# Performance work log

Hardware: AMD Instinct MI355X
Metric: run time of the kernel (lower is better)

Reference implementation:

```python
import jax, jax.numpy as jnp
import numpy as np

B, S, H = 128, 512, 768      # batch, seq, encoder hidden
NL = 42                      # len(LABEL_TO_ID)
LD = 300                     # label_dim
DK, DV = 64, 768             # K_dim, V_dim
HID = 768                    # opt['hidden_dim']
P = 512                      # max_seq_length == pos_indicator
INF = 1e12                   # constant.INFINITY_NUMBER
NEG = -1e9


def gelu(x):
    return 0.5 * x * (1.0 + jax.lax.erf(x * 0.7071067811865476))


def setup_inputs() -> dict:
    key = jax.random.key(0)
    ks = jax.random.split(key, 24)
    sc = 0.02
    return {
        "inputs": jax.random.normal(ks[0], (B, S, H), jnp.float32),
        "pos_ids": jax.random.randint(ks[1], (B, S), 0, 53),
        "dep_ids": jax.random.randint(ks[2], (B, S), 0, 42),
        "subj_pos": jax.random.randint(ks[3], (B, S), 0, P + 1),
        "obj_pos": jax.random.randint(ks[4], (B, S), 0, P + 1),
        "adj": jnp.zeros((1, 1, 1), jnp.float32),  # unused by forward
        # stacked per-label Q/K projections (41 = NL-1 labels, label 0 excluded)
        "WQ": jax.random.normal(ks[5], (NL - 1, DK, H), jnp.float32) * sc,
        "bQ": jax.random.normal(ks[6], (NL - 1, DK), jnp.float32) * sc,
        "WK": jax.random.normal(ks[7], (NL - 1, DK, LD), jnp.float32) * sc,
        "bK": jax.random.normal(ks[8], (NL - 1, DK), jnp.float32) * sc,
        "WV_w": jax.random.normal(ks[9], (DV, H), jnp.float32) * sc,
        "WV_b": jax.random.normal(ks[10], (DV,), jnp.float32) * sc,
        "Wout_w": jax.random.normal(ks[11], (H, DV), jnp.float32) * sc,
        "Wout_b": jax.random.normal(ks[12], (H,), jnp.float32) * sc,
        "ln_g": jnp.ones((H,), jnp.float32),
        "ln_b": jnp.zeros((H,), jnp.float32),
        "label_emb": jax.random.normal(ks[13], (NL, LD), jnp.float32) * sc,
        "feat_w": jax.random.normal(ks[14], (HID, 3 * H), jnp.float32) * sc,
        "feat_b": jax.random.normal(ks[15], (HID,), jnp.float32) * sc,
        "out_w": jax.random.normal(ks[16], (LD, HID), jnp.float32) * sc,
        "out_b": jax.random.normal(ks[17], (LD,), jnp.float32) * sc,
    }


def reference(inputs, pos_ids, dep_ids, subj_pos, obj_pos, adj,
              WQ, bQ, WK, bK, WV_w, WV_b, Wout_w, Wout_b, ln_g, ln_b,
              label_emb, feat_w, feat_b, out_w, out_b):
    dt = inputs.dtype
    # combined attention mask (bool OR, as torch bool+bool): entity markers + padding
    mask = (subj_pos == P) | (obj_pos == P) | (pos_ids == 0)   # [B,S]

    # --- LabelAttention: 41-loop collapses to one fused projection ---
    lab = label_emb[1:NL]                                      # [41,LD] labels 1..41
    kvec = jnp.einsum('ld,lkd->lk', lab, WK) + bK              # [41,DK] per-label keys
    # scores_sum[b,s] = sum_l (x W_Q_l^T + b_Q_l) . k_l  /sqrt(dk)  + 41*mask*NEG
    w_eff = jnp.einsum('lk,lkh->h', kvec, WQ)                  # [H]
    c = jnp.sum(kvec * bQ)                                     # scalar
    scores = (inputs @ w_eff + c) / 8.0                        # sqrt(DK)=8; [B,S]
    scores = scores + (NL - 1) * mask.astype(dt) * NEG
    attn = jax.nn.softmax(scores, axis=-1)                     # [B,S]

    wv = inputs @ WV_w.T + WV_b                                # [B,S,DV]
    ctx = jnp.einsum('bs,bsd->bd', attn, wv)                   # [B,DV]
    ctx = gelu(ctx @ Wout_w.T + Wout_b)                        # [B,H]
    mu = ctx.mean(-1, keepdims=True)
    var = ((ctx - mu) ** 2).mean(-1, keepdims=True)
    ctx = (ctx - mu) / jnp.sqrt(var + 1e-5) * ln_g + ln_b

    # --- entity max pooling (mask True where NOT part of entity) ---
    sm = (subj_pos != P)[:, :, None]
    om = (obj_pos != P)[:, :, None]
    subj_out = jnp.where(sm, -INF, inputs).max(axis=1)         # [B,H]
    obj_out = jnp.where(om, -INF, inputs).max(axis=1)          # [B,H]

    feats = jnp.concatenate([subj_out, obj_out, ctx], axis=-1)  # [B,3H]
    feats = gelu(feats @ feat_w.T + feat_b)                     # [B,HID]
    feats = gelu(feats @ out_w.T + out_b)                       # [B,LD]

    logits = feats @ label_emb.T                                # [B,42]
    return logits, ctx
```

## Files before the change

### kernel.cpp

```cpp
#include <hip/hip_runtime.h>
#include <math.h>

#define BB 128
#define SS 512
#define HH 768
#define PPOS 512
#define NEGC (-1.0e9f)
#define NINF (-1.0e12f)

#define OFF_KVEC   0
#define OFF_WEFF   2624
#define OFF_C      3392
#define OFF_SCORES 4096
#define OFF_CAT    0
#define OFF_POOLED 294912
#define OFF_PP     393216
#define OFF_PS     786432
#define OFF_PO     1179648
#define OFF_CTXA   393216
#define OFF_CTXB   491520
#define OFF_F1     589824
#define OFF_F2     688128

__device__ __forceinline__ float gelu_f(float x) {
    return 0.5f * x * (1.0f + erff(x * 0.70710678118654752f));
}
__device__ __forceinline__ float dot4(float4 a, float4 b) {
    return a.x*b.x + a.y*b.y + a.z*b.z + a.w*b.w;
}

template<int K4, int ACT>
__global__ __launch_bounds__(256) void k_mm(const float* __restrict__ A,
        const float* __restrict__ W, const float* __restrict__ bias,
        float* __restrict__ C, int M, int N) {
    int lane = threadIdx.x & 63;
    int wave = (blockIdx.x * 256 + threadIdx.x) >> 6;
    int ntn = (N + 15) >> 4;
    int m0 = (wave / ntn) << 2;
    if (m0 >= M) return;
    int n0 = ((wave % ntn) << 4) + (lane >> 2);
    int ks = lane & 3;
    bool nvalid = (n0 < N);
    const float4* A4 = (const float4*)A;
    const float4* w_row = (const float4*)W + (size_t)(nvalid ? n0 : 0) * K4;
    const float4* a0 = A4 + (size_t)m0 * K4;
    const float4* a1 = a0 + K4;
    const float4* a2 = a1 + K4;
    const float4* a3 = a2 + K4;
    float acc0 = 0.f, acc1 = 0.f, acc2 = 0.f, acc3 = 0.f;
    #pragma unroll 4
    for (int j = ks; j < K4; j += 4) {
        float4 wv = w_row[j];
        acc0 += dot4(a0[j], wv);
        acc1 += dot4(a1[j], wv);
        acc2 += dot4(a2[j], wv);
        acc3 += dot4(a3[j], wv);
    }
    acc0 += __shfl_xor(acc0, 1, 64); acc0 += __shfl_xor(acc0, 2, 64);
    acc1 += __shfl_xor(acc1, 1, 64); acc1 += __shfl_xor(acc1, 2, 64);
    acc2 += __shfl_xor(acc2, 1, 64); acc2 += __shfl_xor(acc2, 2, 64);
    acc3 += __shfl_xor(acc3, 1, 64); acc3 += __shfl_xor(acc3, 2, 64);
    if (ks == 0 && nvalid) {
        float b = bias ? bias[n0] : 0.f;
        float v0 = acc0 + b, v1 = acc1 + b, v2 = acc2 + b, v3 = acc3 + b;
        if (ACT == 1) { v0 = gelu_f(v0); v1 = gelu_f(v1); v2 = gelu_f(v2); v3 = gelu_f(v3); }
        C[(size_t)m0 * N + n0] = v0;
        C[(size_t)(m0 + 1) * N + n0] = v1;
        C[(size_t)(m0 + 2) * N + n0] = v2;
        C[(size_t)(m0 + 3) * N + n0] = v3;
    }
}

__global__ __launch_bounds__(256) void k_kvec2(const float* __restrict__ label_emb,
        const float* __restrict__ WK, const float* __restrict__ bK,
        float* __restrict__ ws) {
    if (blockIdx.x < 3) ws[OFF_WEFF + blockIdx.x * 256 + threadIdx.x] = 0.f;
    if (blockIdx.x == 3 && threadIdx.x == 0) ws[OFF_C] = 0.f;
    int lane = threadIdx.x & 63;
    int idx = (blockIdx.x * 256 + threadIdx.x) >> 6;
    int l = idx >> 6;
    const float4* lab4 = (const float4*)(label_emb + (size_t)(l + 1) * 300);
    const float4* wk4  = (const float4*)(WK + (size_t)idx * 300);
    float acc = dot4(lab4[lane], wk4[lane]);
    if (lane < 11) acc += dot4(lab4[64 + lane], wk4[64 + lane]);
    #pragma unroll
    for (int off = 32; off > 0; off >>= 1) acc += __shfl_xor(acc, off, 64);
    if (lane == 0) ws[OFF_KVEC + idx] = acc + bK[idx];
}

__global__ __launch_bounds__(256) void k_weff2(const float* __restrict__ WQ,
        const float* __restrict__ bQ, float* __restrict__ ws) {
    int lane = threadIdx.x & 63;
    int w = (blockIdx.x * 256 + threadIdx.x) >> 6;
    if (w < 492) {
        int jc = w / 12, hg = w % 12;
        int h = hg * 64 + lane;
        const float* wq = WQ + (size_t)(jc * 64) * HH + h;
        const float* kv = ws + OFF_KVEC + jc * 64;
        float acc = 0.f;
        #pragma unroll 8
        for (int j = 0; j < 64; ++j) acc += kv[j] * wq[(size_t)j * HH];
        atomicAdd(&ws[OFF_WEFF + h], acc);
    } else if (w == 492) {
        float acc = 0.f;
        for (int j = lane; j < 2624; j += 64) acc += ws[OFF_KVEC + j] * bQ[j];
        #pragma unroll
        for (int off = 32; off > 0; off >>= 1) acc += __shfl_xor(acc, off, 64);
        if (lane == 0) atomicAdd(&ws[OFF_C], acc);
    }
}

__global__ __launch_bounds__(256) void k_scores(const float* __restrict__ inputs,
        const int* __restrict__ pos_ids, const int* __restrict__ subj_pos,
        const int* __restrict__ obj_pos, float* __restrict__ ws) {
    int wave = threadIdx.x >> 6, lane = threadIdx.x & 63;
    const float4* in4 = (const float4*)inputs;
    const float4* w4  = (const float4*)(ws + OFF_WEFF);
    float c = ws[OFF_C];
    float4 w0 = w4[lane], w1 = w4[64 + lane], w2 = w4[128 + lane];
    int wid = blockIdx.x * 4 + wave;
    for (int i = 0; i < 8; ++i) {
        int row = wid + 8192 * i;
        const float4* r4 = in4 + (size_t)row * 192;
        float acc = dot4(r4[lane], w0) + dot4(r4[64 + lane], w1) + dot4(r4[128 + lane], w2);
        #pragma unroll
        for (int off = 32; off > 0; off >>= 1) acc += __shfl_down(acc, off, 64);
        if (lane == 0) {
            bool m = (subj_pos[row] == PPOS) | (obj_pos[row] == PPOS) | (pos_ids[row] == 0);
            float sc = (acc + c) * 0.125f;
            if (m) sc += 41.0f * NEGC;
            ws[OFF_SCORES + row] = sc;
        }
    }
}

__global__ void k_softmax(float* __restrict__ ws) {
    __shared__ float red[256];
    int b = blockIdx.x, t = threadIdx.x;
    float* sc = ws + OFF_SCORES + (size_t)b * SS;
    float v0 = sc[t], v1 = sc[t + 256];
    red[t] = fmaxf(v0, v1); __syncthreads();
    for (int s2 = 128; s2 > 0; s2 >>= 1) {
        if (t < s2) red[t] = fmaxf(red[t], red[t + s2]);
        __syncthreads();
    }
    float m = red[0]; __syncthreads();
    float e0 = expf(v0 - m), e1 = expf(v1 - m);
    red[t] = e0 + e1; __syncthreads();
    for (int s2 = 128; s2 > 0; s2 >>= 1) {
        if (t < s2) red[t] += red[t + s2];
        __syncthreads();
    }
    float inv = 1.0f / red[0];
    sc[t] = e0 * inv; sc[t + 256] = e1 * inv;
}

__global__ __launch_bounds__(192) void k_pool(const float* __restrict__ inputs,
        const int* __restrict__ subj_pos, const int* __restrict__ obj_pos,
        float* __restrict__ ws) {
    __shared__ float la[128];
    __shared__ int lsf[128];
    __shared__ int lof[128];
    int chunk = blockIdx.x, b = blockIdx.y, t = threadIdx.x;
    int s0 = chunk * 128;
    if (t < 128) {
        int gs = b * SS + s0 + t;
        la[t]  = ws[OFF_SCORES + gs];
        lsf[t] = (subj_pos[gs] == PPOS);
        lof[t] = (obj_pos[gs] == PPOS);
    }
    __syncthreads();
    const float4* in4 = (const float4*)inputs;
    float4 pool = make_float4(0.f, 0.f, 0.f, 0.f);
    float4 smax = make_float4(NINF, NINF, NINF, NINF);
    float4 omax = make_float4(NINF, NINF, NINF, NINF);
    for (int s = 0; s < 128; ++s) {
        float4 x = in4[((size_t)(b * SS + s0 + s)) * 192 + t];
        float a = la[s];
        pool.x += a * x.x; pool.y += a * x.y; pool.z += a * x.z; pool.w += a * x.w;
        if (lsf[s]) {
            smax.x = fmaxf(smax.x, x.x); smax.y = fmaxf(smax.y, x.y);
            smax.z = fmaxf(smax.z, x.z); smax.w = fmaxf(smax.w, x.w);
        }
        if (lof[s]) {
            omax.x = fmaxf(omax.x, x.x); omax.y = fmaxf(omax.y, x.y);
            omax.z = fmaxf(omax.z, x.z); omax.w = fmaxf(omax.w, x.w);
        }
    }
    size_t o = (size_t)(b * 4 + chunk) * 192 + t;
    ((float4*)(ws + OFF_PP))[o] = pool;
    ((float4*)(ws + OFF_PS))[o] = smax;
    ((float4*)(ws + OFF_PO))[o] = omax;
}

__global__ void k_reduce(float* __restrict__ ws) {
    int i = blockIdx.x * 256 + threadIdx.x;
    int b = i / HH, h = i - b * HH;
    float p = 0.f, sm = NINF, om = NINF;
    for (int j = 0; j < 4; ++j) {
        int o = (b * 4 + j) * HH + h;
        p += ws[OFF_PP + o];
        sm = fmaxf(sm, ws[OFF_PS + o]);
        om = fmaxf(om, ws[OFF_PO + o]);
    }
    ws[OFF_POOLED + i] = p;
    ws[OFF_CAT + (size_t)b * 2304 + h] = sm;
    ws[OFF_CAT + (size_t)b * 2304 + 768 + h] = om;
}

__global__ void k_ln(const float* __restrict__ ln_g, const float* __restrict__ ln_b,
                     float* __restrict__ ws, float* __restrict__ out) {
    __shared__ float red[256];
    __shared__ float red2[256];
    int b = blockIdx.x, t = threadIdx.x;
    const float* x = ws + OFF_CTXB + (size_t)b * HH;
    float a0 = x[t], a1 = x[t + 256], a2 = x[t + 512];
    red[t]  = a0 + a1 + a2;
    red2[t] = a0 * a0 + a1 * a1 + a2 * a2;
    __syncthreads();
    for (int s2 = 128; s2 > 0; s2 >>= 1) {
        if (t < s2) { red[t] += red[t + s2]; red2[t] += red2[t + s2]; }
        __syncthreads();
    }
    float mu  = red[0] * (1.0f / 768.0f);
    float var = red2[0] * (1.0f / 768.0f) - mu * mu;
    float inv = rsqrtf(var + 1e-5f);
    float* o = out + 5376 + (size_t)b * HH;
    float* cc = ws + OFF_CAT + (size_t)b * 2304 + 1536;
    float r0 = (a0 - mu) * inv * ln_g[t]       + ln_b[t];
    float r1 = (a1 - mu) * inv * ln_g[t + 256] + ln_b[t + 256];
    float r2 = (a2 - mu) * inv * ln_g[t + 512] + ln_b[t + 512];
    o[t] = r0; o[t + 256] = r1; o[t + 512] = r2;
    cc[t] = r0; cc[t + 256] = r1; cc[t + 512] = r2;
}

extern "C" void kernel_launch(void* const* d_in, const int* in_sizes, int n_in,
                              void* d_out, int out_size, void* d_ws, size_t ws_size,
                              hipStream_t stream) {
    const float* inputs    = (const float*)d_in[0];
    const int*   pos_ids   = (const int*)d_in[1];
    const int*   subj_pos  = (const int*)d_in[3];
    const int*   obj_pos   = (const int*)d_in[4];
    const float* WQ        = (const float*)d_in[6];
    const float* bQ        = (const float*)d_in[7];
    const float* WK        = (const float*)d_in[8];
    const float* bK        = (const float*)d_in[9];
    const float* WV_w      = (const float*)d_in[10];
    const float* WV_b      = (const float*)d_in[11];
    const float* Wout_w    = (const float*)d_in[12];
    const float* Wout_b    = (const float*)d_in[13];
    const float* ln_g      = (const float*)d_in[14];
    const float* ln_b      = (const float*)d_in[15];
    const float* label_emb = (const float*)d_in[16];
    const float* feat_w    = (const float*)d_in[17];
    const float* feat_b    = (const float*)d_in[18];
    const float* out_w     = (const float*)d_in[19];
    const float* out_b     = (const float*)d_in[20];
    float* out = (float*)d_out;
    float* ws  = (float*)d_ws;

    k_kvec2  <<<656, 256, 0, stream>>>(label_emb, WK, bK, ws);
    k_weff2  <<<124, 256, 0, stream>>>(WQ, bQ, ws);
    k_scores <<<2048, 256, 0, stream>>>(inputs, pos_ids, subj_pos, obj_pos, ws);
    k_softmax<<<BB, 256, 0, stream>>>(ws);
    k_pool   <<<dim3(4, BB), 192, 0, stream>>>(inputs, subj_pos, obj_pos, ws);
    k_reduce <<<384, 256, 0, stream>>>(ws);
    k_mm<192,0><<<384, 256, 0, stream>>>(ws + OFF_POOLED, WV_w, WV_b, ws + OFF_CTXA, BB, HH);
    k_mm<192,1><<<384, 256, 0, stream>>>(ws + OFF_CTXA, Wout_w, Wout_b, ws + OFF_CTXB, BB, HH);
    k_ln     <<<BB, 256, 0, stream>>>(ln_g, ln_b, ws, out);
    k_mm<576,1><<<384, 256, 0, stream>>>(ws + OFF_CAT, feat_w, feat_b, ws + OFF_F1, BB, HH);
    k_mm<192,1><<<152, 256, 0, stream>>>(ws + OFF_F1, out_w, out_b, ws + OFF_F2, BB, 300);
    k_mm<75,0><<<24, 256, 0, stream>>>(ws + OFF_F2, label_emb, nullptr, out, BB, 42);
}
```

Baseline: 540.0 us.

## Fuse softmax into pooling, split pooling finer, halve matmul row tile

```diff
diff --git a/kernel.cpp b/kernel.cpp
--- a/kernel.cpp
+++ b/kernel.cpp
@@ -15,8 +15,8 @@
 #define OFF_CAT    0
 #define OFF_POOLED 294912
 #define OFF_PP     393216
-#define OFF_PS     786432
-#define OFF_PO     1179648
+#define OFF_PS     1179648
+#define OFF_PO     1966080
 #define OFF_CTXA   393216
 #define OFF_CTXB   491520
 #define OFF_F1     589824
@@ -29,45 +29,43 @@
     return a.x*b.x + a.y*b.y + a.z*b.z + a.w*b.w;
 }
 
-template<int K4, int ACT>
+template<int K4, int ACT, int MT>
 __global__ __launch_bounds__(256) void k_mm(const float* __restrict__ A,
         const float* __restrict__ W, const float* __restrict__ bias,
         float* __restrict__ C, int M, int N) {
     int lane = threadIdx.x & 63;
     int wave = (blockIdx.x * 256 + threadIdx.x) >> 6;
     int ntn = (N + 15) >> 4;
-    int m0 = (wave / ntn) << 2;
+    int m0 = (wave / ntn) * MT;
     if (m0 >= M) return;
     int n0 = ((wave % ntn) << 4) + (lane >> 2);
     int ks = lane & 3;
     bool nvalid = (n0 < N);
     const float4* A4 = (const float4*)A;
     const float4* w_row = (const float4*)W + (size_t)(nvalid ? n0 : 0) * K4;
-    const float4* a0 = A4 + (size_t)m0 * K4;
-    const float4* a1 = a0 + K4;
-    const float4* a2 = a1 + K4;
-    const float4* a3 = a2 + K4;
-    float acc0 = 0.f, acc1 = 0.f, acc2 = 0.f, acc3 = 0.f;
+    const float4* ar = A4 + (size_t)m0 * K4;
+    float acc[MT];
+    #pragma unroll
+    for (int r = 0; r < MT; ++r) acc[r] = 0.f;
     #pragma unroll 4
     for (int j = ks; j < K4; j += 4) {
         float4 wv = w_row[j];
-        acc0 += dot4(a0[j], wv);
-        acc1 += dot4(a1[j], wv);
-        acc2 += dot4(a2[j], wv);
-        acc3 += dot4(a3[j], wv);
-    }
-    acc0 += __shfl_xor(acc0, 1, 64); acc0 += __shfl_xor(acc0, 2, 64);
-    acc1 += __shfl_xor(acc1, 1, 64); acc1 += __shfl_xor(acc1, 2, 64);
-    acc2 += __shfl_xor(acc2, 1, 64); acc2 += __shfl_xor(acc2, 2, 64);
-    acc3 += __shfl_xor(acc3, 1, 64); acc3 += __shfl_xor(acc3, 2, 64);
+        #pragma unroll
+        for (int r = 0; r < MT; ++r) acc[r] += dot4(ar[(size_t)r * K4 + j], wv);
+    }
+    #pragma unroll
+    for (int r = 0; r < MT; ++r) {
+        acc[r] += __shfl_xor(acc[r], 1, 64);
+        acc[r] += __shfl_xor(acc[r], 2, 64);
+    }
     if (ks == 0 && nvalid) {
         float b = bias ? bias[n0] : 0.f;
-        float v0 = acc0 + b, v1 = acc1 + b, v2 = acc2 + b, v3 = acc3 + b;
-        if (ACT == 1) { v0 = gelu_f(v0); v1 = gelu_f(v1); v2 = gelu_f(v2); v3 = gelu_f(v3); }
-        C[(size_t)m0 * N + n0] = v0;
-        C[(size_t)(m0 + 1) * N + n0] = v1;
-        C[(size_t)(m0 + 2) * N + n0] = v2;
-        C[(size_t)(m0 + 3) * N + n0] = v3;
+        #pragma unroll
+        for (int r = 0; r < MT; ++r) {
+            float v = acc[r] + b;
+            if (ACT == 1) v = gelu_f(v);
+            C[(size_t)(m0 + r) * N + n0] = v;
+        }
     }
 }
 
@@ -134,38 +132,39 @@
     }
 }
 
-__global__ void k_softmax(float* __restrict__ ws) {
+__global__ __launch_bounds__(192) void k_pool(const float* __restrict__ inputs,
+        const int* __restrict__ subj_pos, const int* __restrict__ obj_pos,
+        float* __restrict__ ws) {
     __shared__ float red[256];
-    int b = blockIdx.x, t = threadIdx.x;
-    float* sc = ws + OFF_SCORES + (size_t)b * SS;
-    float v0 = sc[t], v1 = sc[t + 256];
-    red[t] = fmaxf(v0, v1); __syncthreads();
+    __shared__ float al[64];
+    __shared__ int lsf[64];
+    __shared__ int lof[64];
+    int chunk = blockIdx.x, b = blockIdx.y, t = threadIdx.x;
+    int s0 = chunk * 64;
+    const float* sc = ws + OFF_SCORES + (size_t)b * SS;
+    float v0 = sc[t], v1 = sc[t + 192], v2 = (t < 128) ? sc[t + 384] : NINF;
+    red[t] = fmaxf(fmaxf(v0, v1), v2);
+    if (t >= 128) { }
+    if (t < 64) red[t + 192] = NINF;
+    __syncthreads();
     for (int s2 = 128; s2 > 0; s2 >>= 1) {
         if (t < s2) red[t] = fmaxf(red[t], red[t + s2]);
         __syncthreads();
     }
-    float m = red[0]; __syncthreads();
-    float e0 = expf(v0 - m), e1 = expf(v1 - m);
-    red[t] = e0 + e1; __syncthreads();
+    float m = red[0];
+    __syncthreads();
+    float e0 = expf(v0 - m) + expf(v1 - m) + ((t < 128) ? expf(v2 - m) : 0.f);
+    red[t] = e0;
+    if (t < 64) red[t + 192] = 0.f;
+    __syncthreads();
     for (int s2 = 128; s2 > 0; s2 >>= 1) {
         if (t < s2) red[t] += red[t + s2];
         __syncthreads();
     }
     float inv = 1.0f / red[0];
-    sc[t] = e0 * inv; sc[t + 256] = e1 * inv;
-}
-
-__global__ __launch_bounds__(192) void k_pool(const float* __restrict__ inputs,
-        const int* __restrict__ subj_pos, const int* __restrict__ obj_pos,
-        float* __restrict__ ws) {
-    __shared__ float la[128];
-    __shared__ int lsf[128];
-    __shared__ int lof[128];
-    int chunk = blockIdx.x, b = blockIdx.y, t = threadIdx.x;
-    int s0 = chunk * 128;
-    if (t < 128) {
+    if (t < 64) {
         int gs = b * SS + s0 + t;
-        la[t]  = ws[OFF_SCORES + gs];
+        al[t]  = expf(sc[s0 + t] - m) * inv;
         lsf[t] = (subj_pos[gs] == PPOS);
         lof[t] = (obj_pos[gs] == PPOS);
     }
@@ -174,9 +173,9 @@
     float4 pool = make_float4(0.f, 0.f, 0.f, 0.f);
     float4 smax = make_float4(NINF, NINF, NINF, NINF);
     float4 omax = make_float4(NINF, NINF, NINF, NINF);
-    for (int s = 0; s < 128; ++s) {
+    for (int s = 0; s < 64; ++s) {
         float4 x = in4[((size_t)(b * SS + s0 + s)) * 192 + t];
-        float a = la[s];
+        float a = al[s];
         pool.x += a * x.x; pool.y += a * x.y; pool.z += a * x.z; pool.w += a * x.w;
         if (lsf[s]) {
             smax.x = fmaxf(smax.x, x.x); smax.y = fmaxf(smax.y, x.y);
@@ -187,7 +186,7 @@
             omax.z = fmaxf(omax.z, x.z); omax.w = fmaxf(omax.w, x.w);
         }
     }
-    size_t o = (size_t)(b * 4 + chunk) * 192 + t;
+    size_t o = (size_t)(b * 8 + chunk) * 192 + t;
     ((float4*)(ws + OFF_PP))[o] = pool;
     ((float4*)(ws + OFF_PS))[o] = smax;
     ((float4*)(ws + OFF_PO))[o] = omax;
@@ -197,8 +196,9 @@
     int i = blockIdx.x * 256 + threadIdx.x;
     int b = i / HH, h = i - b * HH;
     float p = 0.f, sm = NINF, om = NINF;
-    for (int j = 0; j < 4; ++j) {
-        int o = (b * 4 + j) * HH + h;
+    #pragma unroll
+    for (int j = 0; j < 8; ++j) {
+        int o = (b * 8 + j) * HH + h;
         p += ws[OFF_PP + o];
         sm = fmaxf(sm, ws[OFF_PS + o]);
         om = fmaxf(om, ws[OFF_PO + o]);
@@ -262,13 +262,12 @@
     k_kvec2  <<<656, 256, 0, stream>>>(label_emb, WK, bK, ws);
     k_weff2  <<<124, 256, 0, stream>>>(WQ, bQ, ws);
     k_scores <<<2048, 256, 0, stream>>>(inputs, pos_ids, subj_pos, obj_pos, ws);
-    k_softmax<<<BB, 256, 0, stream>>>(ws);
-    k_pool   <<<dim3(4, BB), 192, 0, stream>>>(inputs, subj_pos, obj_pos, ws);
+    k_pool   <<<dim3(8, BB), 192, 0, stream>>>(inputs, subj_pos, obj_pos, ws);
     k_reduce <<<384, 256, 0, stream>>>(ws);
-    k_mm<192,0><<<384, 256, 0, stream>>>(ws + OFF_POOLED, WV_w, WV_b, ws + OFF_CTXA, BB, HH);
-    k_mm<192,1><<<384, 256, 0, stream>>>(ws + OFF_CTXA, Wout_w, Wout_b, ws + OFF_CTXB, BB, HH);
+    k_mm<192,0,2><<<768, 256, 0, stream>>>(ws + OFF_POOLED, WV_w, WV_b, ws + OFF_CTXA, BB, HH);
+    k_mm<192,1,2><<<768, 256, 0, stream>>>(ws + OFF_CTXA, Wout_w, Wout_b, ws + OFF_CTXB, BB, HH);
     k_ln     <<<BB, 256, 0, stream>>>(ln_g, ln_b, ws, out);
-    k_mm<576,1><<<384, 256, 0, stream>>>(ws + OFF_CAT, feat_w, feat_b, ws + OFF_F1, BB, HH);
-    k_mm<192,1><<<152, 256, 0, stream>>>(ws + OFF_F1, out_w, out_b, ws + OFF_F2, BB, 300);
-    k_mm<75,0><<<24, 256, 0, stream>>>(ws + OFF_F2, label_emb, nullptr, out, BB, 42);
-}
+    k_mm<576,1,2><<<768, 256, 0, stream>>>(ws + OFF_CAT, feat_w, feat_b, ws + OFF_F1, BB, HH);
+    k_mm<192,1,2><<<304, 256, 0, stream>>>(ws + OFF_F1, out_w, out_b, ws + OFF_F2, BB, 300);
+    k_mm<75,0,2><<<48, 256, 0, stream>>>(ws + OFF_F2, label_emb, nullptr, out, BB, 42);
+}
```

New measurement: 476.5 us. 11.8% less time.
